# Kernel optimization log

Measured on AMD Instinct MI355X. Metric: run time of the kernel, lower is better.

## Reference

```python
import jax, jax.numpy as jnp
import numpy as np

BN_EPS = 1e-5


def setup_inputs() -> dict:
    key = jax.random.key(0)
    ks = jax.random.split(key, 8)
    B, C, H, W = 8, 256, 64, 64
    Ci = 128
    s_in = 1.0 / np.sqrt(C)
    s_int = 1.0 / np.sqrt(Ci)
    return {
        "x": jax.random.normal(ks[0], (B, C, H, W), jnp.float32),
        "w_g": jax.random.normal(ks[1], (Ci, C), jnp.float32) * s_in,
        "b_g": jnp.zeros((Ci,), jnp.float32),
        "w_theta": jax.random.normal(ks[2], (Ci, C), jnp.float32) * s_in,
        "b_theta": jnp.zeros((Ci,), jnp.float32),
        "w_phi": jax.random.normal(ks[3], (Ci, C), jnp.float32) * s_in,
        "b_phi": jnp.zeros((Ci,), jnp.float32),
        "w_out": jax.random.normal(ks[4], (C, Ci), jnp.float32) * s_int,
        "b_out": jnp.zeros((C,), jnp.float32),
        "bn_gamma": jnp.ones((C,), jnp.float32),
        "bn_beta": jnp.zeros((C,), jnp.float32),
        "bn_mean": jnp.zeros((C,), jnp.float32),
        "bn_var": jnp.ones((C,), jnp.float32),
    }


def reference(x, w_g, b_g, w_theta, b_theta, w_phi, b_phi, w_out, b_out,
              bn_gamma, bn_beta, bn_mean, bn_var):
    B, C, H, W = x.shape
    Ci = w_g.shape[0]
    N = H * W
    # 1x1 convs == per-pixel linear projections
    g = (jnp.einsum('bchw,oc->bhwo', x, w_g) + b_g).reshape(B, N, Ci)
    theta = (jnp.einsum('bchw,oc->bhwo', x, w_theta) + b_theta).reshape(B, N, Ci)
    phi = (jnp.einsum('bchw,oc->bohw', x, w_phi) + b_phi[:, None, None]).reshape(B, Ci, N)
    # full N x N attention (no scaling, as in the original)
    att = jax.nn.softmax(jnp.einsum('bnc,bcm->bnm', theta, phi), axis=-1)
    y = jnp.einsum('bnm,bmc->bnc', att, g).reshape(B, H, W, Ci)
    # output 1x1 conv + inference-mode BatchNorm (per-channel affine)
    out = jnp.einsum('bhwc,oc->bohw', y, w_out) + b_out[:, None, None]
    inv = bn_gamma / jnp.sqrt(bn_var + BN_EPS)
    out = out * inv[:, None, None] + (bn_beta - bn_mean * inv)[:, None, None]
    return x + out
```

## Files before the change

kernel.cpp:

```cpp
#include <hip/hip_runtime.h>
#include <math.h>

#define BB 8
#define CC 256
#define CI 128
#define NN 4096
#define BN_EPS 1e-5f
#define LOG2E 1.4426950408889634f
#define FIXMAX 88.0f

typedef unsigned int uint;
typedef unsigned short ushort;
typedef __bf16 bf16x8 __attribute__((ext_vector_type(8)));
typedef float f32x16 __attribute__((ext_vector_type(16)));

__device__ __forceinline__ ushort bfbits(float f) {
    return __builtin_bit_cast(ushort, (__bf16)f);
}
__device__ __forceinline__ float bf2f(ushort h) {
    return __uint_as_float(((uint)h) << 16);
}
__device__ __forceinline__ uint pk2(float a, float b) {
    return (uint)bfbits(a) | ((uint)bfbits(b) << 16);
}
__device__ __forceinline__ void gload16(const void* g, void* l) {
    __builtin_amdgcn_global_load_lds(
        (const __attribute__((address_space(1))) uint*)g,
        (__attribute__((address_space(3))) uint*)l, 16, 0, 0);
}
__device__ __forceinline__ bf16x8 asbf8(uint4 v) { return __builtin_bit_cast(bf16x8, v); }
__device__ __forceinline__ float fexp2(float a) {
    float e;
    asm("v_exp_f32 %0, %1" : "=v"(e) : "v"(a));
    return e;
}

__global__ __launch_bounds__(256) void wconv_kernel(
    const float* __restrict__ w_t, const float* __restrict__ w_p,
    const float* __restrict__ w_g, const float* __restrict__ w_o,
    const float* __restrict__ bn_g, const float* __restrict__ bn_b,
    const float* __restrict__ bn_m, const float* __restrict__ bn_v,
    const float* __restrict__ b_out,
    uint4* __restrict__ wt_h, uint4* __restrict__ wt_l,
    uint4* __restrict__ wp_h, uint4* __restrict__ wp_l,
    uint4* __restrict__ wg_h, uint4* __restrict__ wg_l,
    uint4* __restrict__ wo_h, uint4* __restrict__ wo_l,
    float* __restrict__ scale, float* __restrict__ shift)
{
    const int t = threadIdx.x, blk = blockIdx.x;
    if (blk == 64) {
        float inv = bn_g[t] * rsqrtf(bn_v[t] + BN_EPS);
        scale[t] = inv;
        shift[t] = b_out[t] * inv + bn_b[t] - bn_m[t] * inv;
        return;
    }
    int u = blk * 256 + t;
    int mat = u >> 12, ul = u & 4095;
    const float* src;
    uint4 *dh, *dl;
    int o, oct, C, O;
    if (mat == 0)      { src = w_t; dh = wt_h; dl = wt_l; }
    else if (mat == 1) { src = w_p; dh = wp_h; dl = wp_l; }
    else if (mat == 2) { src = w_g; dh = wg_h; dl = wg_l; }
    else               { src = w_o; dh = wo_h; dl = wo_l; }
    if (mat < 3) { O = 128; C = 256; o = ul >> 5; oct = ul & 31; }
    else         { O = 256; C = 128; o = ul >> 4; oct = ul & 15; }
    const float* s = src + (size_t)o * C + oct * 8;
    float4 va = *(const float4*)s, vb = *(const float4*)(s + 4);
    float v[8] = {va.x, va.y, va.z, va.w, vb.x, vb.y, vb.z, vb.w};
    uint hw[4], lw[4];
#pragma unroll
    for (int j = 0; j < 4; j++) {
        float a = v[2 * j], c = v[2 * j + 1];
        ushort ha = bfbits(a), hc = bfbits(c);
        hw[j] = (uint)ha | ((uint)hc << 16);
        lw[j] = pk2(a - bf2f(ha), c - bf2f(hc));
    }
    int di = oct * O + o;
    dh[di] = make_uint4(hw[0], hw[1], hw[2], hw[3]);
    dl[di] = make_uint4(lw[0], lw[1], lw[2], lw[3]);
}

__global__ __launch_bounds__(256, 2) void proj3_mfma(
    const float* __restrict__ x,
    const uint4* __restrict__ wt_h, const uint4* __restrict__ wt_l,
    const uint4* __restrict__ wp_h, const uint4* __restrict__ wp_l,
    const uint4* __restrict__ wg_h, const uint4* __restrict__ wg_l,
    const float* __restrict__ b_t, const float* __restrict__ b_p,
    const float* __restrict__ b_g,
    ushort* __restrict__ th_hi, ushort* __restrict__ th_lo,
    ushort* __restrict__ phi, ushort* __restrict__ gT)
{
    __shared__ __align__(16) char xsm[65536];
    const int t  = threadIdx.x;
    const int w  = t >> 6, l = t & 63;
    const int lq = l & 31, h = l >> 5;
    const int b  = blockIdx.x >> 6;
    const int n0 = (blockIdx.x & 63) << 6;

    {
        const int nq = t & 15;
#pragma unroll
        for (int i = 0; i < 2; i++) {
            int oct = (t >> 4) + 16 * i;
            const float* xp = x + ((size_t)b * CC + oct * 8) * NN + n0 + nq * 4;
            float4 r[8];
#pragma unroll
            for (int j = 0; j < 8; j++) r[j] = *(const float4*)(xp + (size_t)j * NN);
#pragma unroll
            for (int k = 0; k < 4; k++) {
                int n = nq * 4 + k;
                float v[8];
#pragma unroll
                for (int j = 0; j < 8; j++) v[j] = ((const float*)&r[j])[k];
                uint hw[4], lw[4];
#pragma unroll
                for (int j = 0; j < 4; j++) {
                    ushort ha = bfbits(v[2 * j]), hc = bfbits(v[2 * j + 1]);
                    hw[j] = (uint)ha | ((uint)hc << 16);
                    lw[j] = pk2(v[2 * j] - bf2f(ha), v[2 * j + 1] - bf2f(hc));
                }
                int uu = oct ^ (n & 31);
                *(uint4*)(xsm + n * 512 + uu * 16) = make_uint4(hw[0], hw[1], hw[2], hw[3]);
                *(uint4*)(xsm + 32768 + n * 512 + uu * 16) = make_uint4(lw[0], lw[1], lw[2], lw[3]);
            }
        }
    }
    __syncthreads();

    const int wo16 = w * 32 + lq;
    f32x16 acc[3][2];
    {
        float bt = b_t[wo16], bp = b_p[wo16];
        acc[0][0] = (f32x16)bt; acc[0][1] = (f32x16)bt;
        acc[1][0] = (f32x16)bp; acc[1][1] = (f32x16)bp;
        acc[2][0] = (f32x16)0.0f; acc[2][1] = (f32x16)0.0f;
    }

#pragma unroll 2
    for (int cs = 0; cs < 16; cs++) {
        int wi = (cs * 2 + h) * 128 + wo16;
        bf16x8 fth = asbf8(wt_h[wi]), ftl = asbf8(wt_l[wi]);
        bf16x8 fph = asbf8(wp_h[wi]), fpl = asbf8(wp_l[wi]);
        bf16x8 fgh = asbf8(wg_h[wi]), fgl = asbf8(wg_l[wi]);
        int xoff = lq * 512 + 16 * ((cs * 2 + h) ^ lq);
        bf16x8 xh0 = asbf8(*(const uint4*)(xsm + xoff));
        bf16x8 xh1 = asbf8(*(const uint4*)(xsm + 16384 + xoff));
        bf16x8 xl0 = asbf8(*(const uint4*)(xsm + 32768 + xoff));
        bf16x8 xl1 = asbf8(*(const uint4*)(xsm + 49152 + xoff));

        acc[0][0] = __builtin_amdgcn_mfma_f32_32x32x16_bf16(xh0, fth, acc[0][0], 0, 0, 0);
        acc[0][0] = __builtin_amdgcn_mfma_f32_32x32x16_bf16(xl0, fth, acc[0][0], 0, 0, 0);
        acc[0][0] = __builtin_amdgcn_mfma_f32_32x32x16_bf16(xh0, ftl, acc[0][0], 0, 0, 0);
        acc[0][1] = __builtin_amdgcn_mfma_f32_32x32x16_bf16(xh1, fth, acc[0][1], 0, 0, 0);
        acc[0][1] = __builtin_amdgcn_mfma_f32_32x32x16_bf16(xl1, fth, acc[0][1], 0, 0, 0);
        acc[0][1] = __builtin_amdgcn_mfma_f32_32x32x16_bf16(xh1, ftl, acc[0][1], 0, 0, 0);

        acc[1][0] = __builtin_amdgcn_mfma_f32_32x32x16_bf16(xh0, fph, acc[1][0], 0, 0, 0);
        acc[1][0] = __builtin_amdgcn_mfma_f32_32x32x16_bf16(xl0, fph, acc[1][0], 0, 0, 0);
        acc[1][0] = __builtin_amdgcn_mfma_f32_32x32x16_bf16(xh0, fpl, acc[1][0], 0, 0, 0);
        acc[1][1] = __builtin_amdgcn_mfma_f32_32x32x16_bf16(xh1, fph, acc[1][1], 0, 0, 0);
        acc[1][1] = __builtin_amdgcn_mfma_f32_32x32x16_bf16(xl1, fph, acc[1][1], 0, 0, 0);
        acc[1][1] = __builtin_amdgcn_mfma_f32_32x32x16_bf16(xh1, fpl, acc[1][1], 0, 0, 0);

        acc[2][0] = __builtin_amdgcn_mfma_f32_32x32x16_bf16(fgh, xh0, acc[2][0], 0, 0, 0);
        acc[2][0] = __builtin_amdgcn_mfma_f32_32x32x16_bf16(fgh, xl0, acc[2][0], 0, 0, 0);
        acc[2][0] = __builtin_amdgcn_mfma_f32_32x32x16_bf16(fgl, xh0, acc[2][0], 0, 0, 0);
        acc[2][1] = __builtin_amdgcn_mfma_f32_32x32x16_bf16(fgh, xh1, acc[2][1], 0, 0, 0);
        acc[2][1] = __builtin_amdgcn_mfma_f32_32x32x16_bf16(fgh, xl1, acc[2][1], 0, 0, 0);
        acc[2][1] = __builtin_amdgcn_mfma_f32_32x32x16_bf16(fgl, xh1, acc[2][1], 0, 0, 0);
    }

#pragma unroll
    for (int ns = 0; ns < 2; ns++) {
        size_t nb = (size_t)b * NN + n0 + ns * 32;
#pragma unroll
        for (int r = 0; r < 16; r++) {
            int nr = (r & 3) + 8 * (r >> 2) + 4 * h;
            size_t idx = (nb + nr) * CI + wo16;
            float tv = acc[0][ns][r] * LOG2E;
            ushort hb = bfbits(tv);
            th_hi[idx] = hb;
            th_lo[idx] = bfbits(tv - bf2f(hb));
            phi[idx]   = bfbits(acc[1][ns][r]);
        }
#pragma unroll
        for (int r = 0; r < 16; r++) {
            int orow = w * 32 + (r & 3) + 8 * (r >> 2) + 4 * h;
            gT[((size_t)b * CI + orow) * NN + n0 + ns * 32 + lq] =
                bfbits(acc[2][ns][r] + b_g[orow]);
        }
    }
}

__global__ __launch_bounds__(512, 2) void attn_mfma(
    const ushort* __restrict__ th_hi, const ushort* __restrict__ th_lo,
    const ushort* __restrict__ phi, const ushort* __restrict__ gT,
    ushort* __restrict__ yh, ushort* __restrict__ yl)
{
    __shared__ __align__(16) char sm[131072];
    const int t    = threadIdx.x;
    const int w    = t >> 6, l = t & 63;
    const int wg   = w & 3, half = w >> 2;
    const int lq   = l & 31, h = l >> 5;
    const int b    = blockIdx.x & 7, qt = blockIdx.x >> 3;
    const int q0   = qt * 128 + wg * 32;

    bf16x8 thh[8], thl[8];
    {
        const char* thp = (const char*)(th_hi + ((size_t)b * NN + q0 + lq) * CI);
        const char* tlp = (const char*)(th_lo + ((size_t)b * NN + q0 + lq) * CI);
#pragma unroll
        for (int cs = 0; cs < 8; cs++) {
            thh[cs] = __builtin_bit_cast(bf16x8, *(const uint4*)(thp + cs * 32 + h * 16));
            thl[cs] = __builtin_bit_cast(bf16x8, *(const uint4*)(tlp + cs * 32 + h * 16));
        }
    }

    const char* phig = (const char*)(phi + (size_t)b * NN * CI);
    const char* gTg  = (const char*)(gT + (size_t)b * NN * CI);
    char* smh = sm + half * 65536;

    f32x16 ya[4];
#pragma unroll
    for (int ct = 0; ct < 4; ct++) ya[ct] = (f32x16)0.0f;
    float l_run = 0.0f;

    auto stage = [&](int buf, int tile) {
        const char* ps = phig + (size_t)tile * 16384;
        const char* gs = gTg + (size_t)tile * 128;
        char* lb = smh + buf * 32768;
#pragma unroll
        for (int j = 0; j < 4; j++) {
            int c  = wg * 4 + j;
            int r  = c * 4 + (l >> 4);
            int cp = ((l & 15) * 16) ^ ((r & 15) << 4);
            gload16(ps + (size_t)r * 256 + cp, lb + c * 1024);
            int r8 = c * 8 + (l >> 3);
            int cg = ((l & 7) * 16) ^ ((r8 & 7) << 4);
            gload16(gs + (size_t)r8 * (NN * 2) + cg, lb + 16384 + c * 1024);
        }
    };

    stage(0, half * 32 + 0);
    stage(1, half * 32 + 1);
    asm volatile("s_waitcnt vmcnt(8)" ::: "memory");
    __builtin_amdgcn_s_barrier();
    __builtin_amdgcn_sched_barrier(0);

    const int swp = (lq & 15) << 4;
    const int swg = (lq & 7) << 4;

    for (int it = 0; it < 32; it++) {
        const char* smb = smh + (it & 1) * 32768;

        f32x16 s0h = (f32x16)0.0f, s0l = (f32x16)0.0f;
        f32x16 s1h = (f32x16)0.0f, s1l = (f32x16)0.0f;
        __builtin_amdgcn_s_setprio(1);
#pragma unroll
        for (int cs = 0; cs < 8; cs++) {
            bf16x8 f0 = __builtin_bit_cast(bf16x8,
                *(const uint4*)(smb + lq * 256 + ((cs * 32 + h * 16) ^ swp)));
            bf16x8 f1 = __builtin_bit_cast(bf16x8,
                *(const uint4*)(smb + (32 + lq) * 256 + ((cs * 32 + h * 16) ^ swp)));
            s0h = __builtin_amdgcn_mfma_f32_32x32x16_bf16(f0, thh[cs], s0h, 0, 0, 0);
            s1h = __builtin_amdgcn_mfma_f32_32x32x16_bf16(f1, thh[cs], s1h, 0, 0, 0);
            s0l = __builtin_amdgcn_mfma_f32_32x32x16_bf16(f0, thl[cs], s0l, 0, 0, 0);
            s1l = __builtin_amdgcn_mfma_f32_32x32x16_bf16(f1, thl[cs], s1l, 0, 0, 0);
        }
        __builtin_amdgcn_s_setprio(0);

        f32x16 sa0 = s0h + s0l, sa1 = s1h + s1l;
        {
            float t0 = 0.f, t1 = 0.f, t2 = 0.f, t3 = 0.f;
#pragma unroll
            for (int r = 0; r < 16; r += 4) {
                sa0[r]     = fexp2(sa0[r] - FIXMAX);     t0 += sa0[r];
                sa0[r + 1] = fexp2(sa0[r + 1] - FIXMAX); t1 += sa0[r + 1];
                sa0[r + 2] = fexp2(sa0[r + 2] - FIXMAX); t2 += sa0[r + 2];
                sa0[r + 3] = fexp2(sa0[r + 3] - FIXMAX); t3 += sa0[r + 3];
            }
#pragma unroll
            for (int r = 0; r < 16; r += 4) {
                sa1[r]     = fexp2(sa1[r] - FIXMAX);     t0 += sa1[r];
                sa1[r + 1] = fexp2(sa1[r + 1] - FIXMAX); t1 += sa1[r + 1];
                sa1[r + 2] = fexp2(sa1[r + 2] - FIXMAX); t2 += sa1[r + 2];
                sa1[r + 3] = fexp2(sa1[r + 3] - FIXMAX); t3 += sa1[r + 3];
            }
            l_run += (t0 + t1) + (t2 + t3);
        }

        __builtin_amdgcn_s_setprio(1);
#pragma unroll
        for (int mt = 0; mt < 2; mt++) {
            const f32x16& pa = mt ? sa1 : sa0;
#pragma unroll
            for (int s = 0; s < 2; s++) {
                const int base = s * 8;
                uint a0 = pk2(pa[base + 0], pa[base + 1]);
                uint a1 = pk2(pa[base + 2], pa[base + 3]);
                uint b0 = pk2(pa[base + 4], pa[base + 5]);
                uint b1 = pk2(pa[base + 6], pa[base + 7]);
                uint xa0 = __shfl_xor(a0, 32), xb0 = __shfl_xor(b0, 32);
                uint xa1 = __shfl_xor(a1, 32), xb1 = __shfl_xor(b1, 32);
                uint4 fw;
                fw.x = h ? xb0 : a0;
                fw.y = h ? xb1 : a1;
                fw.z = h ? b0 : xa0;
                fw.w = h ? b1 : xa1;
                bf16x8 pf = __builtin_bit_cast(bf16x8, fw);
                const int ks = mt * 2 + s;
#pragma unroll
                for (int ct = 0; ct < 4; ct++) {
                    bf16x8 gf = __builtin_bit_cast(bf16x8,
                        *(const uint4*)(smb + 16384 + (ct * 32 + lq) * 128 +
                                        ((ks * 32 + h * 16) ^ swg)));
                    ya[ct] = __builtin_amdgcn_mfma_f32_32x32x16_bf16(gf, pf, ya[ct], 0, 0, 0);
                }
            }
        }
        __builtin_amdgcn_s_setprio(0);

        asm volatile("" ::: "memory");
        __builtin_amdgcn_s_barrier();
        if (it < 30) {
            stage(it & 1, half * 32 + it + 2);
            asm volatile("s_waitcnt vmcnt(8)" ::: "memory");
            __builtin_amdgcn_s_barrier();
            __builtin_amdgcn_sched_barrier(0);
        } else if (it == 30) {
            asm volatile("s_waitcnt vmcnt(0)" ::: "memory");
            __builtin_amdgcn_s_barrier();
            __builtin_amdgcn_sched_barrier(0);
        }
    }

    if (w >= 4) {
        float* dst = (float*)(sm + wg * 16384 + l * 256);
#pragma unroll
        for (int ct = 0; ct < 4; ct++)
#pragma unroll
            for (int r4 = 0; r4 < 4; r4++) {
                int u = (ct * 4 + r4) ^ (l & 15);
                *(float4*)((char*)dst + u * 16) =
                    make_float4(ya[ct][r4 * 4 + 0], ya[ct][r4 * 4 + 1],
                                ya[ct][r4 * 4 + 2], ya[ct][r4 * 4 + 3]);
            }
        ((float*)(sm + 65536))[wg * 64 + l] = l_run;
    }
    __syncthreads();
    if (w < 4) {
        float lself = l_run + __shfl_xor(l_run, 32);
        const float* lBp = (const float*)(sm + 65536) + wg * 64;
        float ltot = lself + lBp[lq] + lBp[lq + 32];
        float inv = 1.0f / ltot;
        const char* src = (const char*)(sm + wg * 16384 + l * 256);
        const size_t qb = ((size_t)b * NN + q0 + lq) * CI;
#pragma unroll
        for (int ct = 0; ct < 4; ct++)
#pragma unroll
            for (int r4 = 0; r4 < 4; r4++) {
                int u = (ct * 4 + r4) ^ (l & 15);
                float4 vB = *(const float4*)(src + u * 16);
                float v0 = (ya[ct][r4 * 4 + 0] + vB.x) * inv;
                float v1 = (ya[ct][r4 * 4 + 1] + vB.y) * inv;
                float v2 = (ya[ct][r4 * 4 + 2] + vB.z) * inv;
                float v3 = (ya[ct][r4 * 4 + 3] + vB.w) * inv;
                ushort h0 = bfbits(v0), h1 = bfbits(v1), h2 = bfbits(v2), h3 = bfbits(v3);
                uint2 hw = make_uint2((uint)h0 | ((uint)h1 << 16),
                                      (uint)h2 | ((uint)h3 << 16));
                uint2 lw = make_uint2(pk2(v0 - bf2f(h0), v1 - bf2f(h1)),
                                      pk2(v2 - bf2f(h2), v3 - bf2f(h3)));
                int co = 32 * ct + 8 * r4 + 4 * h;
                *(uint2*)(yh + qb + co) = hw;
                *(uint2*)(yl + qb + co) = lw;
            }
    }
}

__global__ __launch_bounds__(256, 2) void outproj_mfma(
    const ushort* __restrict__ yh, const ushort* __restrict__ yl,
    const uint4* __restrict__ wo_h, const uint4* __restrict__ wo_l,
    const float* __restrict__ scale, const float* __restrict__ shift,
    const float* __restrict__ x, float* __restrict__ out)
{
    __shared__ __align__(16) char ysm[32768];
    const int t  = threadIdx.x;
    const int w  = t >> 6, l = t & 63;
    const int lq = l & 31, h = l >> 5;
    const int b  = blockIdx.x >> 6;
    const int n0 = (blockIdx.x & 63) << 6;

    {
#pragma unroll
        for (int j = 0; j < 4; j++) {
            int idx = w * 64 + j * 256 + l;
            int row = idx >> 4, u = idx & 15;
            size_t srow = ((size_t)b * NN + n0 + row) * CI;
            int cb = 16 * (u ^ (row & 15));
            gload16((const char*)yh + srow * 2 + cb, ysm + (w * 64 + j * 256) * 16);
            gload16((const char*)yl + srow * 2 + cb, ysm + 16384 + (w * 64 + j * 256) * 16);
        }
    }
    __syncthreads();

#pragma unroll
    for (int oi = 0; oi < 2; oi++) {
        const int ot = w + oi * 4;
        const int ob = ot * 32 + lq;
        f32x16 a0 = (f32x16)0.0f, a1 = (f32x16)0.0f;
#pragma unroll 2
        for (int cs = 0; cs < 8; cs++) {
            int wi = (cs * 2 + h) * 256 + ob;
            bf16x8 wfh = asbf8(wo_h[wi]), wfl = asbf8(wo_l[wi]);
            int xoff = lq * 256 + 16 * ((cs * 2 + h) ^ (lq & 15));
            bf16x8 y0h = asbf8(*(const uint4*)(ysm + xoff));
            bf16x8 y1h = asbf8(*(const uint4*)(ysm + 8192 + xoff));
            bf16x8 y0l = asbf8(*(const uint4*)(ysm + 16384 + xoff));
            bf16x8 y1l = asbf8(*(const uint4*)(ysm + 24576 + xoff));
            a0 = __builtin_amdgcn_mfma_f32_32x32x16_bf16(wfh, y0h, a0, 0, 0, 0);
            a0 = __builtin_amdgcn_mfma_f32_32x32x16_bf16(wfl, y0h, a0, 0, 0, 0);
            a0 = __builtin_amdgcn_mfma_f32_32x32x16_bf16(wfh, y0l, a0, 0, 0, 0);
            a1 = __builtin_amdgcn_mfma_f32_32x32x16_bf16(wfh, y1h, a1, 0, 0, 0);
            a1 = __builtin_amdgcn_mfma_f32_32x32x16_bf16(wfl, y1h, a1, 0, 0, 0);
            a1 = __builtin_amdgcn_mfma_f32_32x32x16_bf16(wfh, y1l, a1, 0, 0, 0);
        }
#pragma unroll
        for (int ns = 0; ns < 2; ns++) {
            const f32x16& av = ns ? a1 : a0;
#pragma unroll
            for (int r = 0; r < 16; r++) {
                int o = ot * 32 + (r & 3) + 8 * (r >> 2) + 4 * h;
                size_t ai = ((size_t)b * CC + o) * NN + n0 + ns * 32 + lq;
                out[ai] = av[r] * scale[o] + shift[o] + x[ai];
            }
        }
    }
}

extern "C" void kernel_launch(void* const* d_in, const int* in_sizes, int n_in,
                              void* d_out, int out_size, void* d_ws, size_t ws_size,
                              hipStream_t stream) {
    const float* x       = (const float*)d_in[0];
    const float* w_g     = (const float*)d_in[1];
    const float* b_g     = (const float*)d_in[2];
    const float* w_theta = (const float*)d_in[3];
    const float* b_theta = (const float*)d_in[4];
    const float* w_phi   = (const float*)d_in[5];
    const float* b_phi   = (const float*)d_in[6];
    const float* w_out   = (const float*)d_in[7];
    const float* b_out   = (const float*)d_in[8];
    const float* bn_g    = (const float*)d_in[9];
    const float* bn_b    = (const float*)d_in[10];
    const float* bn_m    = (const float*)d_in[11];
    const float* bn_v    = (const float*)d_in[12];
    float* out = (float*)d_out;

    const size_t arr = (size_t)BB * NN * CI;
    ushort* th_hi = (ushort*)d_ws;
    ushort* th_lo = th_hi + arr;
    ushort* phiw  = th_lo + arr;
    ushort* gTw   = phiw + arr;
    ushort* yhb   = gTw + arr;
    ushort* ylb   = yhb + arr;
    uint4*  wt_h  = (uint4*)(ylb + arr);
    uint4*  wt_l  = wt_h + 4096;
    uint4*  wp_h  = wt_l + 4096;
    uint4*  wp_l  = wp_h + 4096;
    uint4*  wg_h  = wp_l + 4096;
    uint4*  wg_l  = wg_h + 4096;
    uint4*  wo_h  = wg_l + 4096;
    uint4*  wo_l  = wo_h + 4096;
    float*  scl   = (float*)(wo_l + 4096);
    float*  shf   = scl + 256;

    wconv_kernel<<<65, 256, 0, stream>>>(
        w_theta, w_phi, w_g, w_out, bn_g, bn_b, bn_m, bn_v, b_out,
        wt_h, wt_l, wp_h, wp_l, wg_h, wg_l, wo_h, wo_l, scl, shf);
    proj3_mfma<<<BB * 64, 256, 0, stream>>>(
        x, wt_h, wt_l, wp_h, wp_l, wg_h, wg_l, b_theta, b_phi, b_g,
        th_hi, th_lo, phiw, gTw);
    attn_mfma<<<256, 512, 0, stream>>>(th_hi, th_lo, phiw, gTw, yhb, ylb);
    outproj_mfma<<<BB * 64, 256, 0, stream>>>(
        yhb, ylb, wo_h, wo_l, scl, shf, x, out);
}
```

Baseline: 168.2 us.

## Use single-pass fp16 QK^T instead of split bf16 hi/lo, swap via permlane32

```diff
diff --git a/kernel.cpp b/kernel.cpp
--- a/kernel.cpp
+++ b/kernel.cpp
@@ -12,10 +12,14 @@
 typedef unsigned int uint;
 typedef unsigned short ushort;
 typedef __bf16 bf16x8 __attribute__((ext_vector_type(8)));
+typedef _Float16 f16x8 __attribute__((ext_vector_type(8)));
 typedef float f32x16 __attribute__((ext_vector_type(16)));
 
 __device__ __forceinline__ ushort bfbits(float f) {
     return __builtin_bit_cast(ushort, (__bf16)f);
+}
+__device__ __forceinline__ ushort hbits(float f) {
+    return __builtin_bit_cast(ushort, (_Float16)f);
 }
 __device__ __forceinline__ float bf2f(ushort h) {
     return __uint_as_float(((uint)h) << 16);
@@ -88,8 +92,7 @@
     const uint4* __restrict__ wg_h, const uint4* __restrict__ wg_l,
     const float* __restrict__ b_t, const float* __restrict__ b_p,
     const float* __restrict__ b_g,
-    ushort* __restrict__ th_hi, ushort* __restrict__ th_lo,
-    ushort* __restrict__ phi, ushort* __restrict__ gT)
+    ushort* __restrict__ th, ushort* __restrict__ phi, ushort* __restrict__ gT)
 {
     __shared__ __align__(16) char xsm[65536];
     const int t  = threadIdx.x;
@@ -178,11 +181,8 @@
         for (int r = 0; r < 16; r++) {
             int nr = (r & 3) + 8 * (r >> 2) + 4 * h;
             size_t idx = (nb + nr) * CI + wo16;
-            float tv = acc[0][ns][r] * LOG2E;
-            ushort hb = bfbits(tv);
-            th_hi[idx] = hb;
-            th_lo[idx] = bfbits(tv - bf2f(hb));
-            phi[idx]   = bfbits(acc[1][ns][r]);
+            th[idx]  = hbits(acc[0][ns][r] * LOG2E);
+            phi[idx] = hbits(acc[1][ns][r]);
         }
 #pragma unroll
         for (int r = 0; r < 16; r++) {
@@ -194,8 +194,8 @@
 }
 
 __global__ __launch_bounds__(512, 2) void attn_mfma(
-    const ushort* __restrict__ th_hi, const ushort* __restrict__ th_lo,
-    const ushort* __restrict__ phi, const ushort* __restrict__ gT,
+    const ushort* __restrict__ th, const ushort* __restrict__ phi,
+    const ushort* __restrict__ gT,
     ushort* __restrict__ yh, ushort* __restrict__ yl)
 {
     __shared__ __align__(16) char sm[131072];
@@ -206,15 +206,12 @@
     const int b    = blockIdx.x & 7, qt = blockIdx.x >> 3;
     const int q0   = qt * 128 + wg * 32;
 
-    bf16x8 thh[8], thl[8];
+    f16x8 thf[8];
     {
-        const char* thp = (const char*)(th_hi + ((size_t)b * NN + q0 + lq) * CI);
-        const char* tlp = (const char*)(th_lo + ((size_t)b * NN + q0 + lq) * CI);
-#pragma unroll
-        for (int cs = 0; cs < 8; cs++) {
-            thh[cs] = __builtin_bit_cast(bf16x8, *(const uint4*)(thp + cs * 32 + h * 16));
-            thl[cs] = __builtin_bit_cast(bf16x8, *(const uint4*)(tlp + cs * 32 + h * 16));
-        }
+        const char* thp = (const char*)(th + ((size_t)b * NN + q0 + lq) * CI);
+#pragma unroll
+        for (int cs = 0; cs < 8; cs++)
+            thf[cs] = __builtin_bit_cast(f16x8, *(const uint4*)(thp + cs * 32 + h * 16));
     }
 
     const char* phig = (const char*)(phi + (size_t)b * NN * CI);
@@ -254,23 +251,19 @@
     for (int it = 0; it < 32; it++) {
         const char* smb = smh + (it & 1) * 32768;
 
-        f32x16 s0h = (f32x16)0.0f, s0l = (f32x16)0.0f;
-        f32x16 s1h = (f32x16)0.0f, s1l = (f32x16)0.0f;
+        f32x16 sa0 = (f32x16)0.0f, sa1 = (f32x16)0.0f;
         __builtin_amdgcn_s_setprio(1);
 #pragma unroll
         for (int cs = 0; cs < 8; cs++) {
-            bf16x8 f0 = __builtin_bit_cast(bf16x8,
+            f16x8 f0 = __builtin_bit_cast(f16x8,
                 *(const uint4*)(smb + lq * 256 + ((cs * 32 + h * 16) ^ swp)));
-            bf16x8 f1 = __builtin_bit_cast(bf16x8,
+            f16x8 f1 = __builtin_bit_cast(f16x8,
                 *(const uint4*)(smb + (32 + lq) * 256 + ((cs * 32 + h * 16) ^ swp)));
-            s0h = __builtin_amdgcn_mfma_f32_32x32x16_bf16(f0, thh[cs], s0h, 0, 0, 0);
-            s1h = __builtin_amdgcn_mfma_f32_32x32x16_bf16(f1, thh[cs], s1h, 0, 0, 0);
-            s0l = __builtin_amdgcn_mfma_f32_32x32x16_bf16(f0, thl[cs], s0l, 0, 0, 0);
-            s1l = __builtin_amdgcn_mfma_f32_32x32x16_bf16(f1, thl[cs], s1l, 0, 0, 0);
+            sa0 = __builtin_amdgcn_mfma_f32_32x32x16_f16(f0, thf[cs], sa0, 0, 0, 0);
+            sa1 = __builtin_amdgcn_mfma_f32_32x32x16_f16(f1, thf[cs], sa1, 0, 0, 0);
         }
         __builtin_amdgcn_s_setprio(0);
 
-        f32x16 sa0 = s0h + s0l, sa1 = s1h + s1l;
         {
             float t0 = 0.f, t1 = 0.f, t2 = 0.f, t3 = 0.f;
 #pragma unroll
@@ -301,14 +294,9 @@
                 uint a1 = pk2(pa[base + 2], pa[base + 3]);
                 uint b0 = pk2(pa[base + 4], pa[base + 5]);
                 uint b1 = pk2(pa[base + 6], pa[base + 7]);
-                uint xa0 = __shfl_xor(a0, 32), xb0 = __shfl_xor(b0, 32);
-                uint xa1 = __shfl_xor(a1, 32), xb1 = __shfl_xor(b1, 32);
-                uint4 fw;
-                fw.x = h ? xb0 : a0;
-                fw.y = h ? xb1 : a1;
-                fw.z = h ? b0 : xa0;
-                fw.w = h ? b1 : xa1;
-                bf16x8 pf = __builtin_bit_cast(bf16x8, fw);
+                asm volatile("v_permlane32_swap_b32 %0, %1" : "+v"(a0), "+v"(b0));
+                asm volatile("v_permlane32_swap_b32 %0, %1" : "+v"(a1), "+v"(b1));
+                bf16x8 pf = __builtin_bit_cast(bf16x8, make_uint4(a0, a1, b0, b1));
                 const int ks = mt * 2 + s;
 #pragma unroll
                 for (int ct = 0; ct < 4; ct++) {
@@ -457,9 +445,8 @@
     float* out = (float*)d_out;
 
     const size_t arr = (size_t)BB * NN * CI;
-    ushort* th_hi = (ushort*)d_ws;
-    ushort* th_lo = th_hi + arr;
-    ushort* phiw  = th_lo + arr;
+    ushort* thw   = (ushort*)d_ws;
+    ushort* phiw  = thw + arr;
     ushort* gTw   = phiw + arr;
     ushort* yhb   = gTw + arr;
     ushort* ylb   = yhb + arr;
@@ -479,8 +466,8 @@
         wt_h, wt_l, wp_h, wp_l, wg_h, wg_l, wo_h, wo_l, scl, shf);
     proj3_mfma<<<BB * 64, 256, 0, stream>>>(
         x, wt_h, wt_l, wp_h, wp_l, wg_h, wg_l, b_theta, b_phi, b_g,
-        th_hi, th_lo, phiw, gTw);
-    attn_mfma<<<256, 512, 0, stream>>>(th_hi, th_lo, phiw, gTw, yhb, ylb);
+        thw, phiw, gTw);
+    attn_mfma<<<256, 512, 0, stream>>>(thw, phiw, gTw, yhb, ylb);
     outproj_mfma<<<BB * 64, 256, 0, stream>>>(
         yhb, ylb, wo_h, wo_l, scl, shf, x, out);
 }
```

Result: faster. 140.7 us (-16.3%).
